# Optimization experiments

Hardware: AMD Instinct MI355X
Metric: run time of the kernel (lower is better)

Reference implementation:

```python
import jax, jax.numpy as jnp
import numpy as np

N_NODES = 100000


def _sage_conv(x, edge_index, w_l, w_r, b):
    # PyG SAGEConv (mean aggr, root_weight=True):
    #   out_i = W_l @ mean_{j in N(i)} x_j + b + W_r @ x_i
    # edge_index[0] = source nodes, edge_index[1] = destination nodes.
    src, dst = edge_index[0], edge_index[1]
    msgs = x[src]  # [E, C_in]
    summed = jax.ops.segment_sum(msgs, dst, num_segments=N_NODES)  # [N, C_in]
    deg = jax.ops.segment_sum(jnp.ones((src.shape[0],), x.dtype), dst,
                              num_segments=N_NODES)
    mean = summed / jnp.maximum(deg, 1.0)[:, None]
    return mean @ w_l.T + b + x @ w_r.T


def setup_inputs() -> dict:
    key = jax.random.key(0)
    ks = jax.random.split(key, 12)
    C_IN, C_H, C_OUT = 32, 64, 1
    E = 1600000

    def glorot(k, shape):
        fan_in = shape[1]
        return jax.random.uniform(k, shape, jnp.float32,
                                  -1.0 / np.sqrt(fan_in), 1.0 / np.sqrt(fan_in))

    x = jax.random.normal(ks[0], (N_NODES, C_IN), jnp.float32)
    edge_index = jax.random.randint(ks[1], (2, E), 0, N_NODES, jnp.int64)
    return {
        "x": x,
        "edge_index": edge_index,
        "w_l1": glorot(ks[2], (C_H, C_IN)),
        "w_r1": glorot(ks[3], (C_H, C_IN)),
        "b1": jnp.zeros((C_H,), jnp.float32),
        "w_l2": glorot(ks[4], (C_H, C_H)),
        "w_r2": glorot(ks[5], (C_H, C_H)),
        "b2": jnp.zeros((C_H,), jnp.float32),
        "w_l3": glorot(ks[6], (C_OUT, C_H)),
        "w_r3": glorot(ks[7], (C_OUT, C_H)),
        "b3": jnp.zeros((C_OUT,), jnp.float32),
    }


def reference(x, edge_index, w_l1, w_r1, b1, w_l2, w_r2, b2, w_l3, w_r3, b3):
    h = jax.nn.relu(_sage_conv(x, edge_index, w_l1, w_r1, b1))
    h = jax.nn.relu(_sage_conv(h, edge_index, w_l2, w_r2, b2))
    h = _sage_conv(h, edge_index, w_l3, w_r3, b3)
    return jax.nn.sigmoid(h)
```

## Files before the change

kernel.cpp:

```cpp
#include <hip/hip_runtime.h>
#include <math.h>

#define NN 100000
#define CAP 48
#define ZROW NN
#define XCONV_NB 3125

#define PART_NB 1024
#define STRIDE4 (PART_NB * 256 * 4)
#define BUKN 256
#define NBUK 391
#define LCAPB 4608

typedef float  v4f __attribute__((ext_vector_type(4)));
typedef int    v4i __attribute__((ext_vector_type(4)));

__device__ __forceinline__ unsigned short f2bf(float v) {
    unsigned int u = __float_as_uint(v);
    u += 0x7FFFu + ((u >> 16) & 1u);
    return (unsigned short)(u >> 16);
}
__device__ __forceinline__ float bf2f(unsigned short b) {
    return __uint_as_float(((unsigned int)b) << 16);
}
__device__ __forceinline__ float bflo(unsigned int u) {
    return __uint_as_float(u << 16);
}
__device__ __forceinline__ float bfhi(unsigned int u) {
    return __uint_as_float(u & 0xFFFF0000u);
}
__device__ __forceinline__ unsigned int pack2bf(float a, float b) {
    return (unsigned)f2bf(a) | ((unsigned)f2bf(b) << 16);
}

__global__ __launch_bounds__(256) void part_kernel(
    const int* __restrict__ ei, int* __restrict__ gcur, unsigned int* __restrict__ lists,
    int E, const float* __restrict__ x, unsigned short* __restrict__ xb, int xtotal) {
    if (blockIdx.x >= PART_NB) {
        int i = ((blockIdx.x - PART_NB) * 256 + threadIdx.x) * 4;
        if (i + 3 < xtotal) {
            float4 v = *(const float4*)(x + i);
            ushort4 o;
            o.x = f2bf(v.x); o.y = f2bf(v.y); o.z = f2bf(v.z); o.w = f2bf(v.w);
            *(ushort4*)(xb + i) = o;
        } else {
            for (int j = i; j < xtotal; ++j) xb[j] = f2bf(x[j]);
        }
        return;
    }
    __shared__ int lcnt[NBUK], lbase[NBUK];
    int t = threadIdx.x;
    for (int i = t; i < NBUK; i += 256) lcnt[i] = 0;
    __syncthreads();

    const int* dsts = ei + E;
    unsigned int ent[8];
    int eb[8], rk[8];
    bool val[8];
    int base0 = (blockIdx.x * 256 + t) * 4;

#pragma unroll
    for (int it = 0; it < 2; ++it) {
        int e0 = base0 + it * STRIDE4;
        if (e0 + 3 < E) {
            v4i d = *(const v4i*)(dsts + e0);
            v4i s = *(const v4i*)(ei + e0);
            int dd[4] = {d.x, d.y, d.z, d.w};
            int ss[4] = {s.x, s.y, s.z, s.w};
#pragma unroll
            for (int j = 0; j < 4; ++j) {
                int k = it * 4 + j;
                int b = dd[j] >> 8;
                eb[k] = b;
                ent[k] = ((unsigned int)(dd[j] & 255) << 17) | (unsigned int)ss[j];
                val[k] = true;
                rk[k] = atomicAdd(&lcnt[b], 1);
            }
        } else {
#pragma unroll
            for (int j = 0; j < 4; ++j) {
                int k = it * 4 + j;
                int e = e0 + j;
                val[k] = (e < E);
                eb[k] = 0; ent[k] = 0; rk[k] = 0;
                if (e < E) {
                    int dv = dsts[e];
                    int b = dv >> 8;
                    eb[k] = b;
                    ent[k] = ((unsigned int)(dv & 255) << 17) | (unsigned int)ei[e];
                    rk[k] = atomicAdd(&lcnt[b], 1);
                }
            }
        }
    }
    __syncthreads();
    for (int i = t; i < NBUK; i += 256) lbase[i] = atomicAdd(&gcur[i], lcnt[i]);
    __syncthreads();
#pragma unroll
    for (int k = 0; k < 8; ++k) {
        if (val[k]) {
            int pos = lbase[eb[k]] + rk[k];
            if (pos < LCAPB) lists[(size_t)eb[k] * LCAPB + pos] = ent[k];
        }
    }
}

__global__ __launch_bounds__(256) void fill_kernel(
    const unsigned int* __restrict__ lists, const int* __restrict__ gcur,
    int* __restrict__ cnt, int* __restrict__ csr) {
    __shared__ int lc[BUKN];
    __shared__ int tile[BUKN * CAP];
    int b = blockIdx.x, t = threadIdx.x;
    lc[t] = 0;
    for (int i = t; i < BUKN * CAP; i += 256) tile[i] = ZROW;
    __syncthreads();
    int total = gcur[b];
    if (total > LCAPB) total = LCAPB;
    const unsigned int* lg = lists + (size_t)b * LCAPB;
    for (int e = t; e < total; e += 256) {
        unsigned int ent = lg[e];
        int dl = (int)(ent >> 17);
        int pos = atomicAdd(&lc[dl], 1);
        if (pos < CAP) tile[dl * CAP + pos] = (int)(ent & 0x1FFFFu);
    }
    __syncthreads();
    int nodes = NN - b * BUKN;
    if (nodes > BUKN) nodes = BUKN;
    if (t < nodes) cnt[b * BUKN + t] = lc[t];
    int tot = nodes * CAP;
    int gbase = b * BUKN * CAP;
    for (int i = t * 4; i < tot; i += 1024)
        *(v4i*)(csr + gbase + i) = *(const v4i*)(tile + i);
}


__global__ __launch_bounds__(256) void agg1_kernel(
    const unsigned short* __restrict__ xb, const int* __restrict__ cnt,
    const int* __restrict__ csr, unsigned int* __restrict__ mean1b, int n) {
    int t = threadIdx.x;
    int lane = t & 63, wv = t >> 6;
    int p = lane & 7, q = lane >> 3;
    int ngrp = (n + 3) >> 2;
    for (int grp = blockIdx.x; grp < ngrp; grp += gridDim.x) {
        int node = __builtin_amdgcn_readfirstlane(grp * 4 + wv);
        if (node >= n) continue;
        int deg = cnt[node];
        int len = (deg < CAP) ? deg : CAP;
        int lenp = (len + 15) & ~15;
        int base = node * CAP;
        float aA[4] = {0.f, 0.f, 0.f, 0.f}, aB[4] = {0.f, 0.f, 0.f, 0.f};
        for (int i = 0; i < lenp; i += 16) {
            int i0 = csr[base + i + q];
            int i1 = csr[base + i + 8 + q];
            uint2 uA = *(const uint2*)(xb + (size_t)i0 * 32 + 4 * p);
            uint2 uB = *(const uint2*)(xb + (size_t)i1 * 32 + 4 * p);
            aA[0] += bflo(uA.x); aA[1] += bfhi(uA.x);
            aA[2] += bflo(uA.y); aA[3] += bfhi(uA.y);
            aB[0] += bflo(uB.x); aB[1] += bfhi(uB.x);
            aB[2] += bflo(uB.y); aB[3] += bfhi(uB.y);
        }
        float s[4];
#pragma unroll
        for (int k = 0; k < 4; ++k) {
            float v = aA[k] + aB[k];
            v += __shfl_xor(v, 8, 64);
            v += __shfl_xor(v, 16, 64);
            v += __shfl_xor(v, 32, 64);
            s[k] = v;
        }
        float inv = 1.0f / (float)(deg > 1 ? deg : 1);
        if (q == 0) {
            uint2 o;
            o.x = pack2bf(s[0] * inv, s[1] * inv);
            o.y = pack2bf(s[2] * inv, s[3] * inv);
            *(uint2*)(mean1b + (size_t)node * 16 + p * 2) = o;
        }
    }
}

__global__ __launch_bounds__(256) void agg2_kernel(
    const unsigned short* __restrict__ h1b, const int* __restrict__ cnt,
    const int* __restrict__ csr, unsigned int* __restrict__ mean2b, int n) {
    int t = threadIdx.x;
    int lane = t & 63, wv = t >> 6;
    int p = lane & 15, q = lane >> 4;
    int ngrp = (n + 3) >> 2;
    for (int grp = blockIdx.x; grp < ngrp; grp += gridDim.x) {
        int node = __builtin_amdgcn_readfirstlane(grp * 4 + wv);
        if (node >= n) continue;
        int deg = cnt[node];
        int len = (deg < CAP) ? deg : CAP;
        int lenp = (len + 7) & ~7;
        int base = node * CAP;
        float aA[4] = {0.f, 0.f, 0.f, 0.f}, aB[4] = {0.f, 0.f, 0.f, 0.f};
        for (int i = 0; i < lenp; i += 8) {
            int i0 = csr[base + i + q];
            int i1 = csr[base + i + 4 + q];
            uint2 uA = *(const uint2*)(h1b + (size_t)i0 * 64 + 4 * p);
            uint2 uB = *(const uint2*)(h1b + (size_t)i1 * 64 + 4 * p);
            aA[0] += bflo(uA.x); aA[1] += bfhi(uA.x);
            aA[2] += bflo(uA.y); aA[3] += bfhi(uA.y);
            aB[0] += bflo(uB.x); aB[1] += bfhi(uB.x);
            aB[2] += bflo(uB.y); aB[3] += bfhi(uB.y);
        }
        float s[4];
#pragma unroll
        for (int k = 0; k < 4; ++k) {
            float v = aA[k] + aB[k];
            v += __shfl_xor(v, 16, 64);
            v += __shfl_xor(v, 32, 64);
            s[k] = v;
        }
        float inv = 1.0f / (float)(deg > 1 ? deg : 1);
        if (q == 0) {
            uint2 o;
            o.x = pack2bf(s[0] * inv, s[1] * inv);
            o.y = pack2bf(s[2] * inv, s[3] * inv);
            *(uint2*)(mean2b + (size_t)node * 32 + p * 2) = o;
        }
    }
}

template<int HALF, bool FINAL, bool A1BF>
__global__ __launch_bounds__(256) void lin_kernel(
    const unsigned short* __restrict__ a0b,
    const float* __restrict__ a1f, const unsigned short* __restrict__ a1b,
    const float* __restrict__ w0, const float* __restrict__ w1,
    const float* __restrict__ bias,
    const float* __restrict__ wl3, const float* __restrict__ wr3,
    unsigned short* __restrict__ outb,
    float* __restrict__ z, float* __restrict__ r, int n) {
    const int KC = 32;
    const int K = 2 * HALF;
    __shared__ float A_s[KC * 132];
    __shared__ float B_s[KC * 68];
    int t = threadIdx.x;
    int tx = t & 7;
    int ty = t >> 3;
    int oc0 = tx * 8;
    int node0 = ty * 4;
    int nb = blockIdx.x * 128;
    float acc[4][8];
#pragma unroll
    for (int i = 0; i < 4; ++i)
#pragma unroll
        for (int j = 0; j < 8; ++j) acc[i][j] = 0.f;

    for (int c = 0; c < K / KC; ++c) {
        int koff = c * KC;
        bool useA1 = (koff >= HALF);
        const float* wsrc = useA1 ? w1 : w0;
        int klo = koff % HALF;
        __syncthreads();
        for (int i = t; i < 128 * KC; i += 256) {
            int nd = i >> 5, kk = i & 31;
            int gnode = nb + nd;
            float v = 0.f;
            if (gnode < n) {
                size_t off = (size_t)gnode * HALF + klo + kk;
                if (!useA1) v = bf2f(a0b[off]);
                else v = A1BF ? bf2f(a1b[off]) : a1f[off];
            }
            A_s[kk * 132 + nd] = v;
        }
        for (int i = t; i < 64 * KC; i += 256) {
            int oc = i >> 5, kk = i & 31;
            B_s[kk * 68 + oc] = wsrc[oc * HALF + klo + kk];
        }
        __syncthreads();
#pragma unroll 8
        for (int kk = 0; kk < KC; ++kk) {
            float4 av = *(const float4*)&A_s[kk * 132 + node0];
            float4 b0 = *(const float4*)&B_s[kk * 68 + oc0];
            float4 b1v = *(const float4*)&B_s[kk * 68 + oc0 + 4];
            float aa[4] = {av.x, av.y, av.z, av.w};
            float bb[8] = {b0.x, b0.y, b0.z, b0.w, b1v.x, b1v.y, b1v.z, b1v.w};
#pragma unroll
            for (int i = 0; i < 4; ++i)
#pragma unroll
                for (int j = 0; j < 8; ++j) acc[i][j] += aa[i] * bb[j];
        }
    }

    float bv[8];
#pragma unroll
    for (int j = 0; j < 8; ++j) bv[j] = bias[oc0 + j];

    if (!FINAL) {
#pragma unroll
        for (int i = 0; i < 4; ++i) {
            int node = nb + node0 + i;
            if (node < n) {
                float o[8];
#pragma unroll
                for (int j = 0; j < 8; ++j) o[j] = fmaxf(acc[i][j] + bv[j], 0.f);
                uint4 pk;
                pk.x = pack2bf(o[0], o[1]);
                pk.y = pack2bf(o[2], o[3]);
                pk.z = pack2bf(o[4], o[5]);
                pk.w = pack2bf(o[6], o[7]);
                *(uint4*)&outb[(size_t)node * 64 + oc0] = pk;
            }
        }
    } else {
        float w3l[8], w3r[8];
#pragma unroll
        for (int j = 0; j < 8; ++j) { w3l[j] = wl3[oc0 + j]; w3r[j] = wr3[oc0 + j]; }
#pragma unroll
        for (int i = 0; i < 4; ++i) {
            float zz = 0.f, rr = 0.f;
#pragma unroll
            for (int j = 0; j < 8; ++j) {
                float h2 = fmaxf(acc[i][j] + bv[j], 0.f);
                zz += h2 * w3l[j];
                rr += h2 * w3r[j];
            }
#pragma unroll
            for (int o = 1; o < 8; o <<= 1) {
                zz += __shfl_xor(zz, o, 64);
                rr += __shfl_xor(rr, o, 64);
            }
            int node = nb + node0 + i;
            if (tx == 0 && node < n) { z[node] = zz; r[node] = rr; }
        }
    }
}

__global__ void final_kernel(const float* __restrict__ z, const float* __restrict__ r,
                             const int* __restrict__ cnt, const int* __restrict__ csr,
                             const float* __restrict__ b3, float* __restrict__ out, int n) {
    int t = threadIdx.x;
    int lane = t & 63, wv = t >> 6;
    int node = __builtin_amdgcn_readfirstlane(blockIdx.x * 4 + wv);
    if (node >= n) return;
    int deg = cnt[node];
    int len = (deg < CAP) ? deg : CAP;
    float acc = 0.f;
    if (lane < len) acc = z[csr[node * CAP + lane]];
#pragma unroll
    for (int o = 32; o > 0; o >>= 1) acc += __shfl_down(acc, o, 64);
    if (lane == 0) {
        float m = acc / (float)(deg > 1 ? deg : 1);
        out[node] = 1.0f / (1.0f + expf(-(m + r[node] + b3[0])));
    }
}

extern "C" void kernel_launch(void* const* d_in, const int* in_sizes, int n_in,
                              void* d_out, int out_size, void* d_ws, size_t ws_size,
                              hipStream_t stream) {
    const float* x   = (const float*)d_in[0];
    const int*   ei  = (const int*)d_in[1];
    const float* wl1 = (const float*)d_in[2];
    const float* wr1 = (const float*)d_in[3];
    const float* b1  = (const float*)d_in[4];
    const float* wl2 = (const float*)d_in[5];
    const float* wr2 = (const float*)d_in[6];
    const float* b2  = (const float*)d_in[7];
    const float* wl3 = (const float*)d_in[8];
    const float* wr3 = (const float*)d_in[9];
    const float* b3  = (const float*)d_in[10];
    float* out = (float*)d_out;

    const int E = in_sizes[1] / 2;
    const int n = NN;

    int* cnt = (int*)d_ws;
    int* gcur = cnt + n;
    int* csr = gcur + 392;
    float* z = (float*)(csr + (size_t)n * CAP);
    float* r = z + n;
    unsigned short* xb  = (unsigned short*)(r + n);
    unsigned short* h1b = xb + (size_t)(n + 1) * 32;
    unsigned short* mb  = h1b + (size_t)(n + 1) * 64;
    unsigned int* lists = (unsigned int*)mb;

    hipMemsetAsync(gcur, 0, sizeof(int) * 392, stream);
    hipMemsetAsync(xb + (size_t)n * 32, 0, 64, stream);
    hipMemsetAsync(h1b + (size_t)n * 64, 0, 128, stream);
    part_kernel<<<PART_NB + XCONV_NB, 256, 0, stream>>>(ei, gcur, lists, E, x, xb, n * 32);
    fill_kernel<<<NBUK, 256, 0, stream>>>(lists, gcur, cnt, csr);

    int gemm_grid = (n + 127) / 128;

    agg1_kernel<<<2048, 256, 0, stream>>>(xb, cnt, csr, (unsigned int*)mb, n);
    lin_kernel<32, false, false><<<gemm_grid, 256, 0, stream>>>(
        mb, x, nullptr, wl1, wr1, b1, nullptr, nullptr, h1b, nullptr, nullptr, n);

    agg2_kernel<<<2048, 256, 0, stream>>>(h1b, cnt, csr, (unsigned int*)mb, n);
    lin_kernel<64, true, true><<<gemm_grid, 256, 0, stream>>>(
        mb, nullptr, h1b, wl2, wr2, b2, wl3, wr3, nullptr, z, r, n);

    final_kernel<<<(n + 3) / 4, 256, 0, stream>>>(z, r, cnt, csr, b3, out, n);
}
```

Baseline: 305.5 us.

## Split feature arrays into 16-channel planes and aggregate one plane per block

Node feature tensors (bf16 x and h1) are stored as separate 16-channel planes, 32 bytes per node row, instead of one interleaved row per node. The aggregation kernels become one templated kernel where each block handles a single plane, so each gathered row shrinks and the gathered working set per pass is meant to stay resident in cache. The linear kernels read and write the planar layout. This costs extra CSR index reads, one per plane, and more shuffle reduction steps.

```diff
diff --git a/kernel.cpp b/kernel.cpp
--- a/kernel.cpp
+++ b/kernel.cpp
@@ -12,6 +12,8 @@
 #define NBUK 391
 #define LCAPB 4608
 
+#define RSTRIDE ((size_t)(NN + 1) * 16)
+
 typedef float  v4f __attribute__((ext_vector_type(4)));
 typedef int    v4i __attribute__((ext_vector_type(4)));
 
@@ -35,16 +37,29 @@
 
 __global__ __launch_bounds__(256) void part_kernel(
     const int* __restrict__ ei, int* __restrict__ gcur, unsigned int* __restrict__ lists,
-    int E, const float* __restrict__ x, unsigned short* __restrict__ xb, int xtotal) {
+    int E, const float* __restrict__ x, unsigned short* __restrict__ xh,
+    unsigned short* __restrict__ h1q, int xtotal) {
     if (blockIdx.x >= PART_NB) {
-        int i = ((blockIdx.x - PART_NB) * 256 + threadIdx.x) * 4;
+        int t = threadIdx.x;
+        if (blockIdx.x == PART_NB) {
+            if (t < 64) h1q[(size_t)(t >> 4) * RSTRIDE + (size_t)NN * 16 + (t & 15)] = 0;
+            else if (t < 96) {
+                int u = t - 64;
+                xh[(size_t)(u >> 4) * RSTRIDE + (size_t)NN * 16 + (u & 15)] = 0;
+            }
+        }
+        int i = ((blockIdx.x - PART_NB) * 256 + t) * 4;
         if (i + 3 < xtotal) {
             float4 v = *(const float4*)(x + i);
+            int node = i >> 5, ch = i & 31;
             ushort4 o;
             o.x = f2bf(v.x); o.y = f2bf(v.y); o.z = f2bf(v.z); o.w = f2bf(v.w);
-            *(ushort4*)(xb + i) = o;
+            *(ushort4*)(xh + (size_t)(ch >> 4) * RSTRIDE + (size_t)node * 16 + (ch & 15)) = o;
         } else {
-            for (int j = i; j < xtotal; ++j) xb[j] = f2bf(x[j]);
+            for (int j = i; j < xtotal; ++j) {
+                int node = j >> 5, ch = j & 31;
+                xh[(size_t)(ch >> 4) * RSTRIDE + (size_t)node * 16 + (ch & 15)] = f2bf(x[j]);
+            }
         }
         return;
     }
@@ -133,90 +148,49 @@
         *(v4i*)(csr + gbase + i) = *(const v4i*)(tile + i);
 }
 
-
-__global__ __launch_bounds__(256) void agg1_kernel(
-    const unsigned short* __restrict__ xb, const int* __restrict__ cnt,
-    const int* __restrict__ csr, unsigned int* __restrict__ mean1b, int n) {
+template<int NREGS, int LOG2>
+__global__ __launch_bounds__(256) void agg_kernel(
+    const unsigned short* __restrict__ src,
+    const int* __restrict__ cnt, const int* __restrict__ csr,
+    unsigned int* __restrict__ outb, int n) {
     int t = threadIdx.x;
     int lane = t & 63, wv = t >> 6;
-    int p = lane & 7, q = lane >> 3;
+    int p = lane & 3, e = lane >> 2;
+    int g = blockIdx.x & (NREGS - 1);
+    int bg = blockIdx.x >> LOG2;
+    int nblk = gridDim.x >> LOG2;
+    const unsigned short* sg = src + (size_t)g * RSTRIDE;
     int ngrp = (n + 3) >> 2;
-    for (int grp = blockIdx.x; grp < ngrp; grp += gridDim.x) {
+    for (int grp = bg; grp < ngrp; grp += nblk) {
         int node = __builtin_amdgcn_readfirstlane(grp * 4 + wv);
         if (node >= n) continue;
         int deg = cnt[node];
         int len = (deg < CAP) ? deg : CAP;
         int lenp = (len + 15) & ~15;
         int base = node * CAP;
-        float aA[4] = {0.f, 0.f, 0.f, 0.f}, aB[4] = {0.f, 0.f, 0.f, 0.f};
+        float a[4] = {0.f, 0.f, 0.f, 0.f};
         for (int i = 0; i < lenp; i += 16) {
-            int i0 = csr[base + i + q];
-            int i1 = csr[base + i + 8 + q];
-            uint2 uA = *(const uint2*)(xb + (size_t)i0 * 32 + 4 * p);
-            uint2 uB = *(const uint2*)(xb + (size_t)i1 * 32 + 4 * p);
-            aA[0] += bflo(uA.x); aA[1] += bfhi(uA.x);
-            aA[2] += bflo(uA.y); aA[3] += bfhi(uA.y);
-            aB[0] += bflo(uB.x); aB[1] += bfhi(uB.x);
-            aB[2] += bflo(uB.y); aB[3] += bfhi(uB.y);
+            int idx = csr[base + i + e];
+            uint2 u = *(const uint2*)(sg + (size_t)idx * 16 + p * 4);
+            a[0] += bflo(u.x); a[1] += bfhi(u.x);
+            a[2] += bflo(u.y); a[3] += bfhi(u.y);
         }
         float s[4];
 #pragma unroll
         for (int k = 0; k < 4; ++k) {
-            float v = aA[k] + aB[k];
+            float v = a[k];
+            v += __shfl_xor(v, 4, 64);
             v += __shfl_xor(v, 8, 64);
             v += __shfl_xor(v, 16, 64);
             v += __shfl_xor(v, 32, 64);
             s[k] = v;
         }
         float inv = 1.0f / (float)(deg > 1 ? deg : 1);
-        if (q == 0) {
+        if (e == 0) {
             uint2 o;
             o.x = pack2bf(s[0] * inv, s[1] * inv);
             o.y = pack2bf(s[2] * inv, s[3] * inv);
-            *(uint2*)(mean1b + (size_t)node * 16 + p * 2) = o;
-        }
-    }
-}
-
-__global__ __launch_bounds__(256) void agg2_kernel(
-    const unsigned short* __restrict__ h1b, const int* __restrict__ cnt,
-    const int* __restrict__ csr, unsigned int* __restrict__ mean2b, int n) {
-    int t = threadIdx.x;
-    int lane = t & 63, wv = t >> 6;
-    int p = lane & 15, q = lane >> 4;
-    int ngrp = (n + 3) >> 2;
-    for (int grp = blockIdx.x; grp < ngrp; grp += gridDim.x) {
-        int node = __builtin_amdgcn_readfirstlane(grp * 4 + wv);
-        if (node >= n) continue;
-        int deg = cnt[node];
-        int len = (deg < CAP) ? deg : CAP;
-        int lenp = (len + 7) & ~7;
-        int base = node * CAP;
-        float aA[4] = {0.f, 0.f, 0.f, 0.f}, aB[4] = {0.f, 0.f, 0.f, 0.f};
-        for (int i = 0; i < lenp; i += 8) {
-            int i0 = csr[base + i + q];
-            int i1 = csr[base + i + 4 + q];
-            uint2 uA = *(const uint2*)(h1b + (size_t)i0 * 64 + 4 * p);
-            uint2 uB = *(const uint2*)(h1b + (size_t)i1 * 64 + 4 * p);
-            aA[0] += bflo(uA.x); aA[1] += bfhi(uA.x);
-            aA[2] += bflo(uA.y); aA[3] += bfhi(uA.y);
-            aB[0] += bflo(uB.x); aB[1] += bfhi(uB.x);
-            aB[2] += bflo(uB.y); aB[3] += bfhi(uB.y);
-        }
-        float s[4];
-#pragma unroll
-        for (int k = 0; k < 4; ++k) {
-            float v = aA[k] + aB[k];
-            v += __shfl_xor(v, 16, 64);
-            v += __shfl_xor(v, 32, 64);
-            s[k] = v;
-        }
-        float inv = 1.0f / (float)(deg > 1 ? deg : 1);
-        if (q == 0) {
-            uint2 o;
-            o.x = pack2bf(s[0] * inv, s[1] * inv);
-            o.y = pack2bf(s[2] * inv, s[3] * inv);
-            *(uint2*)(mean2b + (size_t)node * 32 + p * 2) = o;
+            *(uint2*)(outb + (size_t)node * (NREGS * 8) + g * 8 + p * 2) = o;
         }
     }
 }
@@ -257,9 +231,14 @@
             int gnode = nb + nd;
             float v = 0.f;
             if (gnode < n) {
-                size_t off = (size_t)gnode * HALF + klo + kk;
-                if (!useA1) v = bf2f(a0b[off]);
-                else v = A1BF ? bf2f(a1b[off]) : a1f[off];
+                if (!useA1) {
+                    v = bf2f(a0b[(size_t)gnode * HALF + klo + kk]);
+                } else if (A1BF) {
+                    int kabs = klo + kk;
+                    v = bf2f(a1b[(size_t)(kabs >> 4) * RSTRIDE + (size_t)gnode * 16 + (kabs & 15)]);
+                } else {
+                    v = a1f[(size_t)gnode * HALF + klo + kk];
+                }
             }
             A_s[kk * 132 + nd] = v;
         }
@@ -299,7 +278,7 @@
                 pk.y = pack2bf(o[2], o[3]);
                 pk.z = pack2bf(o[4], o[5]);
                 pk.w = pack2bf(o[6], o[7]);
-                *(uint4*)&outb[(size_t)node * 64 + oc0] = pk;
+                *(uint4*)(outb + (size_t)(oc0 >> 4) * RSTRIDE + (size_t)node * 16 + (oc0 & 15)) = pk;
             }
         }
     } else {
@@ -369,26 +348,24 @@
     int* csr = gcur + 392;
     float* z = (float*)(csr + (size_t)n * CAP);
     float* r = z + n;
-    unsigned short* xb  = (unsigned short*)(r + n);
-    unsigned short* h1b = xb + (size_t)(n + 1) * 32;
-    unsigned short* mb  = h1b + (size_t)(n + 1) * 64;
+    unsigned short* xh  = (unsigned short*)(r + n);
+    unsigned short* h1q = xh + 2 * RSTRIDE;
+    unsigned short* mb  = h1q + 4 * RSTRIDE;
     unsigned int* lists = (unsigned int*)mb;
 
     hipMemsetAsync(gcur, 0, sizeof(int) * 392, stream);
-    hipMemsetAsync(xb + (size_t)n * 32, 0, 64, stream);
-    hipMemsetAsync(h1b + (size_t)n * 64, 0, 128, stream);
-    part_kernel<<<PART_NB + XCONV_NB, 256, 0, stream>>>(ei, gcur, lists, E, x, xb, n * 32);
+    part_kernel<<<PART_NB + XCONV_NB, 256, 0, stream>>>(ei, gcur, lists, E, x, xh, h1q, n * 32);
     fill_kernel<<<NBUK, 256, 0, stream>>>(lists, gcur, cnt, csr);
 
     int gemm_grid = (n + 127) / 128;
 
-    agg1_kernel<<<2048, 256, 0, stream>>>(xb, cnt, csr, (unsigned int*)mb, n);
+    agg_kernel<2, 1><<<2048, 256, 0, stream>>>(xh, cnt, csr, (unsigned int*)mb, n);
     lin_kernel<32, false, false><<<gemm_grid, 256, 0, stream>>>(
-        mb, x, nullptr, wl1, wr1, b1, nullptr, nullptr, h1b, nullptr, nullptr, n);
-
-    agg2_kernel<<<2048, 256, 0, stream>>>(h1b, cnt, csr, (unsigned int*)mb, n);
+        mb, x, nullptr, wl1, wr1, b1, nullptr, nullptr, h1q, nullptr, nullptr, n);
+
+    agg_kernel<4, 2><<<2048, 256, 0, stream>>>(h1q, cnt, csr, (unsigned int*)mb, n);
     lin_kernel<64, true, true><<<gemm_grid, 256, 0, stream>>>(
-        mb, nullptr, h1b, wl2, wr2, b2, wl3, wr3, nullptr, z, r, n);
+        mb, nullptr, h1q, wl2, wr2, b2, wl3, wr3, nullptr, z, r, n);
 
     final_kernel<<<(n + 3) / 4, 256, 0, stream>>>(z, r, cnt, csr, b3, out, n);
 }
```

Result: slower. 352.9 us (+15.5%).
